# Performance work log

Measured on AMD Instinct MI355X. Metric: run time of the kernel, lower is better.

Reference implementation:

```python
import jax, jax.numpy as jnp
import numpy as np

B, T, D = 2, 2048, 2048
Q_HEADS, KV_HEADS, HEAD_DIM = 16, 4, 128
ROPE_BASE = 10000.0


def _apply_rotary(x_nhd, positions_n):
    # x_nhd: (N, H, head_dim); half-split rotary embedding.
    half = x_nhd.shape[-1] // 2
    inv_freq = 1.0 / (ROPE_BASE ** (jnp.arange(half, dtype=jnp.float32) / half))
    ang = positions_n.astype(jnp.float32)[:, None] * inv_freq  # (N, half)
    cos = jnp.cos(ang)[:, None, :]  # (N, 1, half)
    sin = jnp.sin(ang)[:, None, :]
    x1, x2 = x_nhd[..., :half], x_nhd[..., half:]
    return jnp.concatenate([x1 * cos - x2 * sin, x1 * sin + x2 * cos], axis=-1)


def setup_inputs() -> dict:
    key = jax.random.key(0)
    ks = jax.random.split(key, 5)
    s_in = 1.0 / np.sqrt(D)
    s_o = 1.0 / np.sqrt(Q_HEADS * HEAD_DIM)
    x = jax.random.normal(ks[0], (B, T, D), dtype=jnp.float32)
    positions = jnp.broadcast_to(jnp.arange(T, dtype=jnp.int32), (B, T))
    wq = jax.random.normal(ks[1], (Q_HEADS * HEAD_DIM, D), dtype=jnp.float32) * s_in
    wk = jax.random.normal(ks[2], (KV_HEADS * HEAD_DIM, D), dtype=jnp.float32) * s_in
    wv = jax.random.normal(ks[3], (KV_HEADS * HEAD_DIM, D), dtype=jnp.float32) * s_in
    wo = jax.random.normal(ks[4], (D, Q_HEADS * HEAD_DIM), dtype=jnp.float32) * s_o
    return {"x": x, "positions": positions, "wq": wq, "wk": wk, "wv": wv, "wo": wo}


def reference(x, positions, wq, wk, wv, wo):
    bsz, tsz, _ = x.shape
    q = jnp.einsum('btd,od->bto', x, wq).reshape(bsz, tsz, Q_HEADS, HEAD_DIM)
    k = jnp.einsum('btd,od->bto', x, wk).reshape(bsz, tsz, KV_HEADS, HEAD_DIM)
    v = jnp.einsum('btd,od->bto', x, wv).reshape(bsz, tsz, KV_HEADS, HEAD_DIM)
    pos_flat = positions.reshape(-1)
    q = _apply_rotary(q.reshape(-1, Q_HEADS, HEAD_DIM), pos_flat).reshape(bsz, tsz, Q_HEADS, HEAD_DIM)
    k = _apply_rotary(k.reshape(-1, KV_HEADS, HEAD_DIM), pos_flat).reshape(bsz, tsz, KV_HEADS, HEAD_DIM)
    rep = Q_HEADS // KV_HEADS
    k = jnp.repeat(k, rep, axis=2)
    v = jnp.repeat(v, rep, axis=2)
    logits = jnp.einsum('bthd,bThd->bhtT', q, k) / jnp.sqrt(jnp.float32(HEAD_DIM))
    causal = jnp.tril(jnp.ones((tsz, tsz), dtype=bool))
    logits = jnp.where(causal[None, None], logits, -1e9)
    weights = jax.nn.softmax(logits, axis=-1)
    ctx = jnp.einsum('bhtT,bThd->bthd', weights, v).reshape(bsz, tsz, Q_HEADS * HEAD_DIM)
    return jnp.einsum('bto,do->btd', ctx, wo)
```

## Files before the change

### kernel.cpp

```cpp
#include <hip/hip_runtime.h>
#include <hip/hip_bf16.h>

typedef __bf16 bf16x8 __attribute__((ext_vector_type(8)));
typedef float  f32x4  __attribute__((ext_vector_type(4)));
typedef float  f32x16 __attribute__((ext_vector_type(16)));

#define B_   2
#define T_   2048
#define D_   2048
#define QH_  16
#define KVH_ 4
#define HD_  128
#define BT_  (B_ * T_)
#define KVD_ 512
#define SCL  0.12751744f

#define GLOAD_LDS16(g, l)                                        \
  __builtin_amdgcn_global_load_lds(                              \
      (const __attribute__((address_space(1))) void*)(g),        \
      (__attribute__((address_space(3))) void*)(l), 16, 0, 0)

__global__ __launch_bounds__(256) void cvt_all(
    const float* __restrict__ x, const float* __restrict__ wq,
    const float* __restrict__ wk, const float* __restrict__ wv,
    const float* __restrict__ wo, ushort* __restrict__ out) {
  const int i = blockIdx.x * 256 + threadIdx.x;
  int j = i;
  const float* src;
  float mul = 1.f;
  if (j < 2097152) { src = x; }
  else if ((j -= 2097152) < 1048576) { src = wq; mul = SCL; }
  else if ((j -= 1048576) < 262144)  { src = wk; }
  else if ((j -= 262144) < 262144)   { src = wv; }
  else { j -= 262144; src = wo; }
  float4 v = ((const float4*)src)[j];
  __hip_bfloat16 h0 = __float2bfloat16(v.x * mul);
  __hip_bfloat16 h1 = __float2bfloat16(v.y * mul);
  __hip_bfloat16 h2 = __float2bfloat16(v.z * mul);
  __hip_bfloat16 h3 = __float2bfloat16(v.w * mul);
  ushort4 o;
  o.x = *(ushort*)&h0; o.y = *(ushort*)&h1;
  o.z = *(ushort*)&h2; o.w = *(ushort*)&h3;
  ((ushort4*)out)[i] = o;
}

__global__ __launch_bounds__(256) void gemm_qkv(
    const ushort* __restrict__ X, const ushort* __restrict__ WQ,
    const ushort* __restrict__ WK, const ushort* __restrict__ WV,
    ushort* __restrict__ qo, ushort* __restrict__ ko, ushort* __restrict__ vo) {
  const int nb = blockIdx.x % 24;
  const int mb = blockIdx.x / 24;
  const int tid = threadIdx.x;
  const int wave = tid >> 6;
  const int lane = tid & 63;
  const int mrow = lane & 15;
  const int quad = lane >> 4;
  const int wm = wave >> 1;
  const int wn = wave & 1;
  const int m0 = mb * 128;
  const int K = D_;

  const ushort* Wg;
  if (nb < 16)      Wg = WQ + (size_t)nb * 128 * K;
  else if (nb < 20) Wg = WK + (size_t)(nb - 16) * 128 * K;
  else              Wg = WV + (size_t)(nb - 20) * 128 * K;

  __shared__ __align__(16) ushort At[128 * 64];
  __shared__ __align__(16) ushort Bt[128 * 64];

  f32x4 acc[4][4];
#pragma unroll
  for (int i = 0; i < 4; ++i)
#pragma unroll
    for (int j = 0; j < 4; ++j) acc[i][j] = (f32x4){0.f, 0.f, 0.f, 0.f};

  const ushort* Xg = X + (size_t)m0 * K;

  for (int k0 = 0; k0 < K; k0 += 64) {
#pragma unroll
    for (int p = 0; p < 4; ++p) {
      const int c = p * 256 + tid;
      const int row = c >> 3;
      const int cc = (c & 7) ^ (row & 7);
      GLOAD_LDS16(Xg + (size_t)row * K + k0 + cc * 8,
                  At + (size_t)(p * 256 + wave * 64) * 8);
      GLOAD_LDS16(Wg + (size_t)row * K + k0 + cc * 8,
                  Bt + (size_t)(p * 256 + wave * 64) * 8);
    }
    __syncthreads();

#pragma unroll
    for (int s = 0; s < 2; ++s) {
      bf16x8 af[4], bfr[4];
#pragma unroll
      for (int mt = 0; mt < 4; ++mt) {
        const int row = wm * 64 + mt * 16 + mrow;
        af[mt] = *reinterpret_cast<const bf16x8*>(
            At + row * 64 + (((s * 4 + quad) ^ (row & 7)) * 8));
      }
#pragma unroll
      for (int nt = 0; nt < 4; ++nt) {
        const int row = wn * 64 + nt * 16 + mrow;
        bfr[nt] = *reinterpret_cast<const bf16x8*>(
            Bt + row * 64 + (((s * 4 + quad) ^ (row & 7)) * 8));
      }
#pragma unroll
      for (int mt = 0; mt < 4; ++mt)
#pragma unroll
        for (int nt = 0; nt < 4; ++nt)
          acc[mt][nt] = __builtin_amdgcn_mfma_f32_16x16x32_bf16(
              af[mt], bfr[nt], acc[mt][nt], 0, 0, 0);
    }
    __syncthreads();
  }

#pragma unroll
  for (int mt = 0; mt < 4; ++mt) {
#pragma unroll
    for (int nt = 0; nt < 4; ++nt) {
      const int colw = wn * 64 + nt * 16 + mrow;
      const int row0 = m0 + wm * 64 + mt * 16 + quad * 4;
      if (nb < 16) {
        const int col = nb * 128 + colw;
#pragma unroll
        for (int r = 0; r < 4; ++r) {
          __hip_bfloat16 hh = __float2bfloat16(acc[mt][nt][r]);
          qo[(size_t)(row0 + r) * 2048 + col] = *(ushort*)&hh;
        }
      } else if (nb < 20) {
        const int col = (nb - 16) * 128 + colw;
#pragma unroll
        for (int r = 0; r < 4; ++r) {
          __hip_bfloat16 hh = __float2bfloat16(acc[mt][nt][r]);
          ko[(size_t)(row0 + r) * KVD_ + col] = *(ushort*)&hh;
        }
      } else {
        const int col = (nb - 20) * 128 + colw;
        const int bb = row0 >> 11;
        const int t0 = row0 & (T_ - 1);
        ushort4 s4;
#pragma unroll
        for (int r = 0; r < 4; ++r) {
          __hip_bfloat16 hh = __float2bfloat16(acc[mt][nt][r]);
          (&s4.x)[r] = *(ushort*)&hh;
        }
        *(ushort4*)(vo + ((size_t)(bb * KVD_ + col)) * T_ + t0) = s4;
      }
    }
  }
}

__global__ __launch_bounds__(256) void gemm_o(
    const ushort* __restrict__ X, const ushort* __restrict__ W,
    float* __restrict__ Y, int M, int N, int K) {
  const int nb128 = N >> 7;
  const int mb = blockIdx.x / nb128;
  const int nb = blockIdx.x % nb128;
  const int tid = threadIdx.x;
  const int wave = tid >> 6;
  const int lane = tid & 63;
  const int mrow = lane & 15;
  const int quad = lane >> 4;
  const int wm = wave >> 1;
  const int wn = wave & 1;
  const int m0 = mb * 128;
  const int n0 = nb * 128;

  __shared__ __align__(16) ushort At[128 * 64];
  __shared__ __align__(16) ushort Bt[128 * 64];

  f32x4 acc[4][4];
#pragma unroll
  for (int i = 0; i < 4; ++i)
#pragma unroll
    for (int j = 0; j < 4; ++j) acc[i][j] = (f32x4){0.f, 0.f, 0.f, 0.f};

  const ushort* Xg = X + (size_t)m0 * K;
  const ushort* Wg = W + (size_t)n0 * K;

  for (int k0 = 0; k0 < K; k0 += 64) {
#pragma unroll
    for (int p = 0; p < 4; ++p) {
      const int c = p * 256 + tid;
      const int row = c >> 3;
      const int cc = (c & 7) ^ (row & 7);
      GLOAD_LDS16(Xg + (size_t)row * K + k0 + cc * 8,
                  At + (size_t)(p * 256 + wave * 64) * 8);
      GLOAD_LDS16(Wg + (size_t)row * K + k0 + cc * 8,
                  Bt + (size_t)(p * 256 + wave * 64) * 8);
    }
    __syncthreads();

#pragma unroll
    for (int s = 0; s < 2; ++s) {
      bf16x8 af[4], bfr[4];
#pragma unroll
      for (int mt = 0; mt < 4; ++mt) {
        const int row = wm * 64 + mt * 16 + mrow;
        af[mt] = *reinterpret_cast<const bf16x8*>(
            At + row * 64 + (((s * 4 + quad) ^ (row & 7)) * 8));
      }
#pragma unroll
      for (int nt = 0; nt < 4; ++nt) {
        const int row = wn * 64 + nt * 16 + mrow;
        bfr[nt] = *reinterpret_cast<const bf16x8*>(
            Bt + row * 64 + (((s * 4 + quad) ^ (row & 7)) * 8));
      }
#pragma unroll
      for (int mt = 0; mt < 4; ++mt)
#pragma unroll
        for (int nt = 0; nt < 4; ++nt)
          acc[mt][nt] = __builtin_amdgcn_mfma_f32_16x16x32_bf16(
              af[mt], bfr[nt], acc[mt][nt], 0, 0, 0);
    }
    __syncthreads();
  }

#pragma unroll
  for (int mt = 0; mt < 4; ++mt)
#pragma unroll
    for (int nt = 0; nt < 4; ++nt) {
      const int col = n0 + wn * 64 + nt * 16 + mrow;
      const int row0 = m0 + wm * 64 + mt * 16 + quad * 4;
#pragma unroll
      for (int r = 0; r < 4; ++r)
        Y[(size_t)(row0 + r) * N + col] = acc[mt][nt][r];
    }
}

__global__ __launch_bounds__(256) void rope_kernel(
    __hip_bfloat16* __restrict__ q, __hip_bfloat16* __restrict__ k,
    const int* __restrict__ positions) {
  const int wave = threadIdx.x >> 6;
  const int lane = threadIdx.x & 63;
  const int p = blockIdx.x * 4 + wave;
  const int head = p % (QH_ + KVH_);
  const int bt = p / (QH_ + KVH_);

  __hip_bfloat16* base;
  if (head < QH_) base = q + ((size_t)bt * QH_ + head) * HD_;
  else            base = k + ((size_t)bt * KVH_ + (head - QH_)) * HD_;

  const float pos = (float)positions[bt];
  const float inv_freq = exp2f((float)lane * -0.20762050593f);
  const float ang = pos * inv_freq;
  const float c = cosf(ang);
  const float s = sinf(ang);

  const float x1 = __bfloat162float(base[lane]);
  const float x2 = __bfloat162float(base[lane + 64]);
  base[lane]      = __float2bfloat16(x1 * c - x2 * s);
  base[lane + 64] = __float2bfloat16(x1 * s + x2 * c);
}

__global__ __launch_bounds__(256, 2) void attn_mfma(
    const ushort* __restrict__ q, const ushort* __restrict__ k,
    const ushort* __restrict__ vt, ushort* __restrict__ ctx) {
  const int tid = threadIdx.x;
  const int wave = tid >> 6;
  const int lane = tid & 63;
  const int m5 = lane & 31;
  const int hi = lane >> 5;

  int i = blockIdx.x;
  int bh, qt;
  if (i < 256) { bh = i >> 5; qt = 63 - (i & 31); }
  else { i -= 256; bh = i >> 5; qt = i & 31; }
  const int hkv = bh & 3;
  const int b   = bh >> 2;
  const int h   = hkv * 4 + wave;
  const int q0  = qt * 32;

  __shared__ __align__(16) ushort kt[2][64 * 128];
  __shared__ __align__(16) ushort vtile[2][128 * 64];
  __shared__ __align__(16) ushort pbuf[4][32 * 64];
  ushort* pw = pbuf[wave];

  const ushort* qrow =
      q + ((size_t)(b * T_ + q0 + m5) * QH_ + h) * HD_ + hi * 8;
  bf16x8 qf[8];
#pragma unroll
  for (int c = 0; c < 8; ++c)
    qf[c] = *reinterpret_cast<const bf16x8*>(qrow + c * 16);

  f32x16 o4[4];
#pragma unroll
  for (int dt = 0; dt < 4; ++dt)
#pragma unroll
    for (int r = 0; r < 16; ++r) o4[dt][r] = 0.f;
  f32x16 ls;
#pragma unroll
  for (int r = 0; r < 16; ++r) ls[r] = 0.f;
  bf16x8 ones;
#pragma unroll
  for (int e = 0; e < 8; ++e) ones[e] = (__bf16)1.0f;

  const ushort* kbase = k + ((size_t)b * T_ * KVH_ + hkv) * HD_;
  const ushort* vbase = vt + (size_t)(b * KVD_ + hkv * HD_) * T_;

  const int nblk = (q0 + 32 + 63) >> 6;

#pragma unroll
  for (int p = 0; p < 4; ++p) {
    const int c = p * 256 + tid;
    const int krow = c >> 4;
    const int kco = (c & 15) ^ (krow & 15);
    GLOAD_LDS16(kbase + (size_t)krow * KVD_ + kco * 8,
                kt[0] + (size_t)(p * 256 + wave * 64) * 8);
    const int vrow = c >> 3;
    const int vco = (c & 7) ^ (vrow & 7);
    GLOAD_LDS16(vbase + (size_t)vrow * T_ + vco * 8,
                vtile[0] + (size_t)(p * 256 + wave * 64) * 8);
  }
  __syncthreads();

  for (int blk = 0; blk < nblk; ++blk) {
    const int cur = blk & 1;
    const int j0 = blk * 64;

    if (blk + 1 < nblk) {
      const int j1 = j0 + 64;
#pragma unroll
      for (int p = 0; p < 4; ++p) {
        const int c = p * 256 + tid;
        const int krow = c >> 4;
        const int kco = (c & 15) ^ (krow & 15);
        GLOAD_LDS16(kbase + (size_t)(j1 + krow) * KVD_ + kco * 8,
                    kt[cur ^ 1] + (size_t)(p * 256 + wave * 64) * 8);
        const int vrow = c >> 3;
        const int vco = (c & 7) ^ (vrow & 7);
        GLOAD_LDS16(vbase + (size_t)vrow * T_ + j1 + vco * 8,
                    vtile[cur ^ 1] + (size_t)(p * 256 + wave * 64) * 8);
      }
    }

    const ushort* pk = kt[cur];
    const ushort* pv = vtile[cur];

#pragma unroll
    for (int t2 = 0; t2 < 2; ++t2) {
      f32x16 sa;
#pragma unroll
      for (int r = 0; r < 16; ++r) sa[r] = 0.f;
      const int rowk = t2 * 32 + m5;
#pragma unroll
      for (int c = 0; c < 8; ++c) {
        const int chunk = (2 * c + hi) ^ (rowk & 15);
        bf16x8 kf =
            *reinterpret_cast<const bf16x8*>(pk + rowk * 128 + chunk * 8);
        sa = __builtin_amdgcn_mfma_f32_32x32x16_bf16(qf[c], kf, sa, 0, 0, 0);
      }
      const int kk = t2 * 32 + m5;
      if (blk == nblk - 1) {
#pragma unroll
        for (int reg = 0; reg < 16; ++reg) {
          const int qrw = (reg & 3) + 8 * (reg >> 2) + 4 * hi;
          const float p = (j0 + kk > q0 + qrw) ? 0.f : exp2f(sa[reg]);
          __hip_bfloat16 hb = __float2bfloat16(p);
          pw[qrw * 64 + (((kk >> 3) ^ (qrw & 7)) * 8) + (kk & 7)] =
              *(ushort*)&hb;
        }
      } else {
#pragma unroll
        for (int reg = 0; reg < 16; ++reg) {
          const int qrw = (reg & 3) + 8 * (reg >> 2) + 4 * hi;
          const float p = exp2f(sa[reg]);
          __hip_bfloat16 hb = __float2bfloat16(p);
          pw[qrw * 64 + (((kk >> 3) ^ (qrw & 7)) * 8) + (kk & 7)] =
              *(ushort*)&hb;
        }
      }
    }

#pragma unroll
    for (int c = 0; c < 4; ++c) {
      const int rowp = m5;
      const int chp = (2 * c + hi) ^ (rowp & 7);
      bf16x8 pa =
          *reinterpret_cast<const bf16x8*>(pw + rowp * 64 + chp * 8);
      ls = __builtin_amdgcn_mfma_f32_32x32x16_bf16(pa, ones, ls, 0, 0, 0);
#pragma unroll
      for (int dt = 0; dt < 4; ++dt) {
        const int rowv = dt * 32 + m5;
        const int chv = (2 * c + hi) ^ (rowv & 7);
        bf16x8 vf =
            *reinterpret_cast<const bf16x8*>(pv + rowv * 64 + chv * 8);
        o4[dt] = __builtin_amdgcn_mfma_f32_32x32x16_bf16(pa, vf, o4[dt], 0, 0, 0);
      }
    }

    __syncthreads();
  }

#pragma unroll
  for (int reg = 0; reg < 16; ++reg) {
    const int qrw = (reg & 3) + 8 * (reg >> 2) + 4 * hi;
    const float rl = 1.f / ls[reg];
    ushort* op =
        ctx + ((size_t)(b * T_ + q0 + qrw) * QH_ + h) * HD_ + m5;
#pragma unroll
    for (int dt = 0; dt < 4; ++dt) {
      __hip_bfloat16 hb = __float2bfloat16(o4[dt][reg] * rl);
      op[dt * 32] = *(ushort*)&hb;
    }
  }
}

extern "C" void kernel_launch(void* const* d_in, const int* in_sizes, int n_in,
                              void* d_out, int out_size, void* d_ws, size_t ws_size,
                              hipStream_t stream) {
  const float* x  = (const float*)d_in[0];
  const int* pos  = (const int*)d_in[1];
  const float* wq = (const float*)d_in[2];
  const float* wk = (const float*)d_in[3];
  const float* wv = (const float*)d_in[4];
  const float* wo = (const float*)d_in[5];

  ushort* xb  = (ushort*)d_ws;
  ushort* wqb = xb  + (size_t)8388608;
  ushort* wkb = wqb + (size_t)4194304;
  ushort* wvb = wkb + (size_t)1048576;
  ushort* wob = wvb + (size_t)1048576;
  ushort* qb  = wob + (size_t)4194304;
  ushort* kb  = qb  + (size_t)8388608;
  ushort* vtb = kb  + (size_t)2097152;
  ushort* ctx = xb;

  cvt_all<<<18432, 256, 0, stream>>>(x, wq, wk, wv, wo, (ushort*)d_ws);

  gemm_qkv<<<(BT_ / 128) * 24, 256, 0, stream>>>(xb, wqb, wkb, wvb, qb, kb, vtb);

  rope_kernel<<<(BT_ * (QH_ + KVH_)) / 4, 256, 0, stream>>>(
      (__hip_bfloat16*)qb, (__hip_bfloat16*)kb, pos);

  attn_mfma<<<512, 256, 0, stream>>>(qb, kb, vtb, ctx);

  gemm_o<<<(BT_ / 128) * (D_ / 128), 256, 0, stream>>>(
      ctx, wob, (float*)d_out, BT_, D_, QH_ * HD_);
}
```

Baseline: 329.7 us.

## Compute transposed scores and keep P in registers via permlane swap

Swaps the MFMA operand order so the score tile comes out transposed (keys in rows, queries in lanes). The probabilities can then be packed to bf16 and rearranged with permlane32 swaps into the A-operand layout for the PV MFMA, with no round trip through the per-wave LDS buffer. The row-sum is accumulated in scalar registers with a final cross-lane shuffle, replacing the MFMA against a ones vector. QK is also split into two independent accumulators to shorten the dependency chain, at the cost of extra registers and shuffles.

```diff
diff --git a/kernel.cpp b/kernel.cpp
--- a/kernel.cpp
+++ b/kernel.cpp
@@ -4,6 +4,7 @@
 typedef __bf16 bf16x8 __attribute__((ext_vector_type(8)));
 typedef float  f32x4  __attribute__((ext_vector_type(4)));
 typedef float  f32x16 __attribute__((ext_vector_type(16)));
+typedef unsigned int u32x2 __attribute__((ext_vector_type(2)));
 
 #define B_   2
 #define T_   2048
@@ -253,6 +254,26 @@
   base[lane + 64] = __float2bfloat16(x1 * s + x2 * c);
 }
 
+static __device__ __forceinline__ unsigned pk2(float a, float b) {
+  __hip_bfloat16 ha = __float2bfloat16(a);
+  __hip_bfloat16 hb = __float2bfloat16(b);
+  return (unsigned)(*(ushort*)&ha) | ((unsigned)(*(ushort*)&hb) << 16);
+}
+
+static __device__ __forceinline__ void hswap(unsigned& a, unsigned& b,
+                                             const int hi) {
+#if __has_builtin(__builtin_amdgcn_permlane32_swap)
+  u32x2 r = __builtin_amdgcn_permlane32_swap(a, b, false, false);
+  a = r.x;
+  b = r.y;
+#else
+  unsigned s = __shfl_xor(hi ? a : b, 32, 64);
+  unsigned na = hi ? s : a;
+  b = hi ? b : s;
+  a = na;
+#endif
+}
+
 __global__ __launch_bounds__(256, 2) void attn_mfma(
     const ushort* __restrict__ q, const ushort* __restrict__ k,
     const ushort* __restrict__ vt, ushort* __restrict__ ctx) {
@@ -273,8 +294,6 @@
 
   __shared__ __align__(16) ushort kt[2][64 * 128];
   __shared__ __align__(16) ushort vtile[2][128 * 64];
-  __shared__ __align__(16) ushort pbuf[4][32 * 64];
-  ushort* pw = pbuf[wave];
 
   const ushort* qrow =
       q + ((size_t)(b * T_ + q0 + m5) * QH_ + h) * HD_ + hi * 8;
@@ -288,12 +307,7 @@
   for (int dt = 0; dt < 4; ++dt)
 #pragma unroll
     for (int r = 0; r < 16; ++r) o4[dt][r] = 0.f;
-  f32x16 ls;
-#pragma unroll
-  for (int r = 0; r < 16; ++r) ls[r] = 0.f;
-  bf16x8 ones;
-#pragma unroll
-  for (int e = 0; e < 8; ++e) ones[e] = (__bf16)1.0f;
+  float ls = 0.f;
 
   const ushort* kbase = k + ((size_t)b * T_ * KVH_ + hkv) * HD_;
   const ushort* vbase = vt + (size_t)(b * KVD_ + hkv * HD_) * T_;
@@ -334,68 +348,78 @@
       }
     }
 
-    const ushort* pk = kt[cur];
+    const ushort* pk_ = kt[cur];
     const ushort* pv = vtile[cur];
 
 #pragma unroll
     for (int t2 = 0; t2 < 2; ++t2) {
-      f32x16 sa;
-#pragma unroll
-      for (int r = 0; r < 16; ++r) sa[r] = 0.f;
+      f32x16 sa0, sa1;
+#pragma unroll
+      for (int r = 0; r < 16; ++r) { sa0[r] = 0.f; sa1[r] = 0.f; }
       const int rowk = t2 * 32 + m5;
 #pragma unroll
-      for (int c = 0; c < 8; ++c) {
-        const int chunk = (2 * c + hi) ^ (rowk & 15);
-        bf16x8 kf =
-            *reinterpret_cast<const bf16x8*>(pk + rowk * 128 + chunk * 8);
-        sa = __builtin_amdgcn_mfma_f32_32x32x16_bf16(qf[c], kf, sa, 0, 0, 0);
-      }
-      const int kk = t2 * 32 + m5;
+      for (int c = 0; c < 8; c += 2) {
+        const int ch0 = (2 * c + hi) ^ (rowk & 15);
+        bf16x8 kf0 =
+            *reinterpret_cast<const bf16x8*>(pk_ + rowk * 128 + ch0 * 8);
+        sa0 = __builtin_amdgcn_mfma_f32_32x32x16_bf16(kf0, qf[c], sa0, 0, 0, 0);
+        const int ch1 = (2 * (c + 1) + hi) ^ (rowk & 15);
+        bf16x8 kf1 =
+            *reinterpret_cast<const bf16x8*>(pk_ + rowk * 128 + ch1 * 8);
+        sa1 = __builtin_amdgcn_mfma_f32_32x32x16_bf16(kf1, qf[c + 1], sa1,
+                                                      0, 0, 0);
+      }
+      f32x16 sa = sa0 + sa1;
+
+      float p[16];
       if (blk == nblk - 1) {
 #pragma unroll
-        for (int reg = 0; reg < 16; ++reg) {
-          const int qrw = (reg & 3) + 8 * (reg >> 2) + 4 * hi;
-          const float p = (j0 + kk > q0 + qrw) ? 0.f : exp2f(sa[reg]);
-          __hip_bfloat16 hb = __float2bfloat16(p);
-          pw[qrw * 64 + (((kk >> 3) ^ (qrw & 7)) * 8) + (kk & 7)] =
-              *(ushort*)&hb;
+        for (int r = 0; r < 16; ++r) {
+          const int key = j0 + t2 * 32 + (r & 3) + 8 * (r >> 2) + 4 * hi;
+          p[r] = (key > q0 + m5) ? 0.f : exp2f(sa[r]);
         }
       } else {
 #pragma unroll
-        for (int reg = 0; reg < 16; ++reg) {
-          const int qrw = (reg & 3) + 8 * (reg >> 2) + 4 * hi;
-          const float p = exp2f(sa[reg]);
-          __hip_bfloat16 hb = __float2bfloat16(p);
-          pw[qrw * 64 + (((kk >> 3) ^ (qrw & 7)) * 8) + (kk & 7)] =
-              *(ushort*)&hb;
+        for (int r = 0; r < 16; ++r) p[r] = exp2f(sa[r]);
+      }
+#pragma unroll
+      for (int r = 0; r < 16; ++r) ls += p[r];
+
+      unsigned u0 = pk2(p[0], p[1]),   u1 = pk2(p[2], p[3]);
+      unsigned u2 = pk2(p[4], p[5]),   u3 = pk2(p[6], p[7]);
+      unsigned u4 = pk2(p[8], p[9]),   u5 = pk2(p[10], p[11]);
+      unsigned u6 = pk2(p[12], p[13]), u7 = pk2(p[14], p[15]);
+      hswap(u0, u2, hi); hswap(u1, u3, hi);
+      hswap(u4, u6, hi); hswap(u5, u7, hi);
+
+#pragma unroll
+      for (int half = 0; half < 2; ++half) {
+        union { unsigned w[4]; bf16x8 v; } pa;
+        pa.w[0] = half ? u4 : u0;
+        pa.w[1] = half ? u5 : u1;
+        pa.w[2] = half ? u6 : u2;
+        pa.w[3] = half ? u7 : u3;
+        const int c = t2 * 2 + half;
+#pragma unroll
+        for (int dt = 0; dt < 4; ++dt) {
+          const int rowv = dt * 32 + m5;
+          const int chv = (2 * c + hi) ^ (rowv & 7);
+          bf16x8 vf =
+              *reinterpret_cast<const bf16x8*>(pv + rowv * 64 + chv * 8);
+          o4[dt] =
+              __builtin_amdgcn_mfma_f32_32x32x16_bf16(pa.v, vf, o4[dt], 0, 0, 0);
         }
       }
     }
 
-#pragma unroll
-    for (int c = 0; c < 4; ++c) {
-      const int rowp = m5;
-      const int chp = (2 * c + hi) ^ (rowp & 7);
-      bf16x8 pa =
-          *reinterpret_cast<const bf16x8*>(pw + rowp * 64 + chp * 8);
-      ls = __builtin_amdgcn_mfma_f32_32x32x16_bf16(pa, ones, ls, 0, 0, 0);
-#pragma unroll
-      for (int dt = 0; dt < 4; ++dt) {
-        const int rowv = dt * 32 + m5;
-        const int chv = (2 * c + hi) ^ (rowv & 7);
-        bf16x8 vf =
-            *reinterpret_cast<const bf16x8*>(pv + rowv * 64 + chv * 8);
-        o4[dt] = __builtin_amdgcn_mfma_f32_32x32x16_bf16(pa, vf, o4[dt], 0, 0, 0);
-      }
-    }
-
     __syncthreads();
   }
 
+  const float lt = ls + __shfl_xor(ls, 32, 64);
 #pragma unroll
   for (int reg = 0; reg < 16; ++reg) {
     const int qrw = (reg & 3) + 8 * (reg >> 2) + 4 * hi;
-    const float rl = 1.f / ls[reg];
+    const float rl = 1.f / __shfl(lt, qrw, 64);
     ushort* op =
         ctx + ((size_t)(b * T_ + q0 + qrw) * QH_ + h) * HD_ + m5;
 #pragma unroll
```

After: 326.2 us. No clear change (-1.1%).
